# Kernel optimization log

Measured on AMD Instinct MI355X. Metric: run time of the kernel, lower is better.

## Reference

```python
import jax, jax.numpy as jnp
import numpy as np

NUM_EXPERTS = 64
TOP_K = 2
DIM = 4096
TOKENS = 16384


def setup_inputs() -> dict:
    key = jax.random.key(0)
    k1, k2 = jax.random.split(key)
    x = jax.random.normal(k1, (TOKENS, DIM), dtype=jnp.float32)
    # nn.Linear weight: [num_experts, dim], scaled like kaiming-uniform-ish init
    w_gating = jax.random.normal(k2, (NUM_EXPERTS, DIM), dtype=jnp.float32) * (1.0 / np.sqrt(DIM))
    return {"x": x, "w_gating": w_gating}


def reference(x, w_gating):
    # gating linear (no bias, noise=0 / eval mode)
    logits = jnp.einsum("td,ed->te", x, w_gating)          # [tokens, experts]
    scores = jax.nn.softmax(logits, axis=-1)                # [tokens, experts]
    topk_scores, topk_experts = jax.lax.top_k(scores, TOP_K)  # [tokens, top_k]
    combine_weight = topk_scores
    me = scores.mean(axis=0)                                # [experts]
    ce = (scores > 0).astype(jnp.float32).mean(axis=0)      # [experts]
    load_balance_loss = (me * ce).sum() * NUM_EXPERTS
    z_loss = (jax.nn.logsumexp(logits, axis=-1) ** 2).mean()
    return topk_experts, combine_weight, scores, load_balance_loss, z_loss
```

## Files before the change

### kernel.cpp

```cpp
#include <hip/hip_runtime.h>
#include <hip/hip_bf16.h>

typedef __attribute__((ext_vector_type(8))) short bf16x8;
typedef __attribute__((ext_vector_type(4))) float f32x4;

#define N_TOKENS 16384
#define DIM 4096
#define TOKB 32
#define NIT 32
#define NBUF 4
#define BUF_F (16 * 256)
#define N_EXP 64

#define OFF_W   (N_TOKENS * 2)
#define OFF_S   (N_TOKENS * 4)
#define OFF_LBL (N_TOKENS * 4 + N_TOKENS * N_EXP)
#define OFF_Z   (OFF_LBL + 1)

#define WS_WHI_F 512
#define WS_WLO_F (512 + (N_EXP * DIM) / 2)

typedef const __attribute__((address_space(1))) void GV;
typedef __attribute__((address_space(3))) void LV;

__device__ __forceinline__ unsigned int pkhi(float a, float b) {
  return __builtin_amdgcn_perm(__float_as_uint(b), __float_as_uint(a), 0x07060302u);
}
__device__ __forceinline__ float resid(float f) {
  return f - __uint_as_float(__float_as_uint(f) & 0xFFFF0000u);
}
__device__ __forceinline__ void tsplit8(const f32x4 p0, const f32x4 p1,
                                        bf16x8& hi, bf16x8& lo) {
  uint4 H = make_uint4(pkhi(p0[0], p0[1]), pkhi(p0[2], p0[3]),
                       pkhi(p1[0], p1[1]), pkhi(p1[2], p1[3]));
  float r0 = resid(p0[0]), r1 = resid(p0[1]), r2 = resid(p0[2]), r3 = resid(p0[3]);
  float r4 = resid(p1[0]), r5 = resid(p1[1]), r6 = resid(p1[2]), r7 = resid(p1[3]);
  uint4 L = make_uint4(pkhi(r0, r1), pkhi(r2, r3), pkhi(r4, r5), pkhi(r6, r7));
  hi = __builtin_bit_cast(bf16x8, H);
  lo = __builtin_bit_cast(bf16x8, L);
}

__global__ __launch_bounds__(256) void split_w_kernel(
    const float* __restrict__ w,
    unsigned short* __restrict__ whi, unsigned short* __restrict__ wlo)
{
  const int i = blockIdx.x * 256 + threadIdx.x;
  const int e = i >> 12, k = i & 4095;
  float f = w[i];
  unsigned short h = __builtin_bit_cast(unsigned short, __float2bfloat16(f));
  float hf = __uint_as_float(((unsigned)h) << 16);
  unsigned short l = __builtin_bit_cast(unsigned short, __float2bfloat16(f - hf));
  const int q = e >> 5, n = (e >> 4) & 1, r15 = e & 15;
  const int kc = k >> 8, kq = (k >> 6) & 3, j = (k >> 5) & 1, half = (k >> 3) & 3,
            jj = k & 7;
  const int lane = half * 16 + r15;
  const int idx = ((kq * 2 + q) << 15) + kc * 2048 + (j * 2 + n) * 512 + lane * 8 + jj;
  whi[idx] = h;
  wlo[idx] = l;
}

__global__ __launch_bounds__(512, 4) void router_kernel(
    const float* __restrict__ x,
    const unsigned short* __restrict__ whi, const unsigned short* __restrict__ wlo,
    float* __restrict__ out, float* __restrict__ ws)
{
  __shared__ __align__(16) float smem[NBUF * BUF_F];

  const int tid  = threadIdx.x;
  const int lane = tid & 63;
  const int wv   = __builtin_amdgcn_readfirstlane(tid >> 6);
  const int q    = wv & 1;
  const int kq   = wv >> 1;
  const int half = lane >> 4;
  const int r15  = lane & 15;
  const int g8   = r15 & 7;
  const int tok0 = blockIdx.x * TOKB;

  const int rl0 = 2 * wv, rl1 = 2 * wv + 1;
  const float* gs00 = x + (size_t)(tok0 + rl0) * DIM      + ((lane ^ (rl0 & 7)) << 2);
  const float* gs01 = x + (size_t)(tok0 + rl1) * DIM      + ((lane ^ (rl1 & 7)) << 2);
  const float* gs10 = x + (size_t)(tok0 + 16 + rl0) * DIM + ((lane ^ (rl0 & 7)) << 2);
  const float* gs11 = x + (size_t)(tok0 + 16 + rl1) * DIM + ((lane ^ (rl1 & 7)) << 2);
  float* const ldst = smem + wv * 512;

#define STAGE(buf, it_) do {                                                  \
    const int rh_ = (it_) & 1;                                                \
    const size_t ko_ = (size_t)((it_) >> 1) * 256;                            \
    const float* s0_ = (rh_ ? gs10 : gs00) + ko_;                             \
    const float* s1_ = (rh_ ? gs11 : gs01) + ko_;                             \
    float* d_ = ldst + (buf) * BUF_F;                                         \
    __builtin_amdgcn_global_load_lds((GV*)s0_, (LV*)d_,       16, 0, 0);      \
    __builtin_amdgcn_global_load_lds((GV*)s1_, (LV*)(d_+256), 16, 0, 0);      \
  } while (0)

  const unsigned short* wph = whi + ((kq * 2 + q) << 15);
  const unsigned short* wpl = wlo + ((kq * 2 + q) << 15);
  const int lo16 = lane * 8;

  f32x4 acc0[2], acc1[2];
#pragma unroll
  for (int n = 0; n < 2; ++n) {
    acc0[n] = (f32x4){0.f, 0.f, 0.f, 0.f};
    acc1[n] = (f32x4){0.f, 0.f, 0.f, 0.f};
  }

#define COMPUTE(itc, ACC, H00, H01, H10, H11, L00, L01, L10, L11) do {         \
    const float* rp = smem + ((itc) & 3) * BUF_F + r15 * 256;                  \
     {                                                              \
      const int u0 = kq * 16 + ((half * 2) ^ g8);                              \
      const int u1 = kq * 16 + ((half * 2 + 1) ^ g8);                          \
      f32x4 p0 = *(const f32x4*)(rp + (u0 << 2));                              \
      f32x4 p1 = *(const f32x4*)(rp + (u1 << 2));                              \
      bf16x8 ah, al;                                                           \
      tsplit8(p0, p1, ah, al);                                                 \
      ACC[0] = __builtin_amdgcn_mfma_f32_16x16x32_bf16(ah, H00, ACC[0], 0, 0, 0); \
      ACC[0] = __builtin_amdgcn_mfma_f32_16x16x32_bf16(al, H00, ACC[0], 0, 0, 0); \
      ACC[0] = __builtin_amdgcn_mfma_f32_16x16x32_bf16(ah, L00, ACC[0], 0, 0, 0); \
      ACC[1] = __builtin_amdgcn_mfma_f32_16x16x32_bf16(ah, H01, ACC[1], 0, 0, 0); \
      ACC[1] = __builtin_amdgcn_mfma_f32_16x16x32_bf16(al, H01, ACC[1], 0, 0, 0); \
      ACC[1] = __builtin_amdgcn_mfma_f32_16x16x32_bf16(ah, L01, ACC[1], 0, 0, 0); \
    }                                                                          \
     {                                                              \
      const int u0 = kq * 16 + 8 + ((half * 2) ^ g8);                          \
      const int u1 = kq * 16 + 8 + ((half * 2 + 1) ^ g8);                      \
      f32x4 p0 = *(const f32x4*)(rp + (u0 << 2));                              \
      f32x4 p1 = *(const f32x4*)(rp + (u1 << 2));                              \
      bf16x8 ah, al;                                                           \
      tsplit8(p0, p1, ah, al);                                                 \
      ACC[0] = __builtin_amdgcn_mfma_f32_16x16x32_bf16(ah, H10, ACC[0], 0, 0, 0); \
      ACC[0] = __builtin_amdgcn_mfma_f32_16x16x32_bf16(al, H10, ACC[0], 0, 0, 0); \
      ACC[0] = __builtin_amdgcn_mfma_f32_16x16x32_bf16(ah, L10, ACC[0], 0, 0, 0); \
      ACC[1] = __builtin_amdgcn_mfma_f32_16x16x32_bf16(ah, H11, ACC[1], 0, 0, 0); \
      ACC[1] = __builtin_amdgcn_mfma_f32_16x16x32_bf16(al, H11, ACC[1], 0, 0, 0); \
      ACC[1] = __builtin_amdgcn_mfma_f32_16x16x32_bf16(ah, L11, ACC[1], 0, 0, 0); \
    }                                                                          \
  } while (0)

  STAGE(0, 0);
  STAGE(1, 1);

  for (int s = 0; s < NIT / 2; ++s) {
    const int it0 = 2 * s, it1 = 2 * s + 1;

    const unsigned short* ph = wph + s * 2048;
    const unsigned short* pl = wpl + s * 2048;
    bf16x8 H00 = *(const bf16x8*)(ph + lo16);
    bf16x8 H01 = *(const bf16x8*)(ph + 512 + lo16);
    bf16x8 H10 = *(const bf16x8*)(ph + 1024 + lo16);
    bf16x8 H11 = *(const bf16x8*)(ph + 1536 + lo16);
    bf16x8 L00 = *(const bf16x8*)(pl + lo16);
    bf16x8 L01 = *(const bf16x8*)(pl + 512 + lo16);
    bf16x8 L10 = *(const bf16x8*)(pl + 1024 + lo16);
    bf16x8 L11 = *(const bf16x8*)(pl + 1536 + lo16);

    STAGE((it0 + 2) & 3, (it0 + 2 < NIT) ? it0 + 2 : NIT - 1);

    asm volatile("s_waitcnt vmcnt(12)" ::: "memory");
    __builtin_amdgcn_s_barrier();
    COMPUTE(it0, acc0, H00, H01, H10, H11, L00, L01, L10, L11);

    STAGE((it1 + 2) & 3, (it1 + 2 < NIT) ? it1 + 2 : NIT - 1);
    asm volatile("s_waitcnt vmcnt(4)" ::: "memory");
    __builtin_amdgcn_s_barrier();
    COMPUTE(it1, acc1, H00, H01, H10, H11, L00, L01, L10, L11);
  }

  asm volatile("s_waitcnt vmcnt(0)" ::: "memory");
  __syncthreads();

  float* lb = smem;
  {
    float* dst = lb + kq * (TOKB * 65);
#pragma unroll
    for (int n = 0; n < 2; ++n) {
#pragma unroll
      for (int r = 0; r < 4; ++r) {
        dst[(half * 4 + r) * 65 + q * 32 + n * 16 + r15]      = acc0[n][r];
        dst[(16 + half * 4 + r) * 65 + q * 32 + n * 16 + r15] = acc1[n][r];
      }
    }
  }
  __syncthreads();

  for (int i = tid; i < TOKB * 64; i += 512) {
    const int t = i >> 6, e = i & 63;
    lb[t * 65 + e] += lb[2080 + t * 65 + e] + lb[4160 + t * 65 + e] + lb[6240 + t * 65 + e];
  }
  __syncthreads();

  if (wv == 0 && lane < TOKB) {
    const int token = tok0 + lane;
    float v[64];
#pragma unroll
    for (int e = 0; e < 64; ++e) v[e] = lb[lane * 65 + e];
    float m = v[0];
#pragma unroll
    for (int e = 1; e < 64; ++e) m = fmaxf(m, v[e]);
    float sum = 0.f;
#pragma unroll
    for (int e = 0; e < 64; ++e) { v[e] = expf(v[e] - m); sum += v[e]; }
    const float inv = 1.0f / sum;
    float m1 = -1.f, m2 = -1.f;
    int   i1 = 0,    i2 = 0;
#pragma unroll
    for (int e = 0; e < 64; ++e) {
      float sc = v[e] * inv;
      lb[lane * 65 + e] = sc;
      if (sc > m1)      { m2 = m1; i2 = i1; m1 = sc; i1 = e; }
      else if (sc > m2) { m2 = sc; i2 = e; }
    }
    out[2 * token]         = (float)i1;
    out[2 * token + 1]     = (float)i2;
    out[OFF_W + 2 * token]     = m1;
    out[OFF_W + 2 * token + 1] = m2;

    float lse = m + logf(sum);
    float z = lse * lse;
#pragma unroll
    for (int off = 16; off > 0; off >>= 1) z += __shfl_down(z, off);
    if (lane == 0) atomicAdd(ws + 128, z);
  }
  __syncthreads();

  float* outS = out + OFF_S + (size_t)blockIdx.x * TOKB * 64;
  for (int i = tid; i < TOKB * 64; i += 512) {
    outS[i] = lb[(i >> 6) * 65 + (i & 63)];
  }

  if (wv == 0) {
    float sm = 0.f, cn = 0.f;
#pragma unroll
    for (int t = 0; t < TOKB; ++t) {
      float sc = lb[t * 65 + lane];
      sm += sc;
      cn += (sc > 0.f) ? 1.f : 0.f;
    }
    atomicAdd(ws + lane, sm);
    atomicAdd(ws + 64 + lane, cn);
  }
#undef STAGE
#undef COMPUTE
}

__global__ void finalize_kernel(const float* __restrict__ ws, float* __restrict__ out) {
  const int l = threadIdx.x;
  const float invT = 1.0f / (float)N_TOKENS;
  float me = ws[l] * invT;
  float ce = ws[64 + l] * invT;
  float p = me * ce;
#pragma unroll
  for (int off = 32; off > 0; off >>= 1) p += __shfl_down(p, off);
  if (l == 0) {
    out[OFF_LBL] = p * (float)N_EXP;
    out[OFF_Z]   = ws[128] * invT;
  }
}

extern "C" void kernel_launch(void* const* d_in, const int* in_sizes, int n_in,
                              void* d_out, int out_size, void* d_ws, size_t ws_size,
                              hipStream_t stream) {
  const float* x = (const float*)d_in[0];
  const float* w = (const float*)d_in[1];
  float* out = (float*)d_out;
  float* ws  = (float*)d_ws;
  unsigned short* whi = (unsigned short*)(ws + WS_WHI_F);
  unsigned short* wlo = (unsigned short*)(ws + WS_WLO_F);

  (void)hipMemsetAsync(d_ws, 0, 129 * sizeof(float), stream);
  split_w_kernel<<<(N_EXP * DIM) / 256, 256, 0, stream>>>(w, whi, wlo);
  router_kernel<<<N_TOKENS / TOKB, 512, 0, stream>>>(x, whi, wlo, out, ws);
  finalize_kernel<<<1, 64, 0, stream>>>(ws, out);
}
```

Before: 81.78 us.

## Fuse memset and finalize into kernels, vectorize weight split

Removes the hipMemsetAsync by zeroing the accumulator workspace inside split_w_kernel, and removes the finalize kernel by having the last router block (detected via an atomic counter) compute the load-balance and z losses. split_w_kernel now processes 8 weights per thread with vector loads and 16-byte stores. This cuts two launches and makes the weight split more memory-efficient, at the cost of an extra barrier and an atomic per router block.

New measurement: 92.33 us. 12.9% more time.

```diff
diff --git a/kernel.cpp b/kernel.cpp
--- a/kernel.cpp
+++ b/kernel.cpp
@@ -11,6 +11,7 @@
 #define NBUF 4
 #define BUF_F (16 * 256)
 #define N_EXP 64
+#define NBLK (N_TOKENS / TOKB)
 
 #define OFF_W   (N_TOKENS * 2)
 #define OFF_S   (N_TOKENS * 4)
@@ -42,21 +43,35 @@
 
 __global__ __launch_bounds__(256) void split_w_kernel(
     const float* __restrict__ w,
-    unsigned short* __restrict__ whi, unsigned short* __restrict__ wlo)
+    unsigned short* __restrict__ whi, unsigned short* __restrict__ wlo,
+    float* __restrict__ ws)
 {
-  const int i = blockIdx.x * 256 + threadIdx.x;
-  const int e = i >> 12, k = i & 4095;
-  float f = w[i];
-  unsigned short h = __builtin_bit_cast(unsigned short, __float2bfloat16(f));
-  float hf = __uint_as_float(((unsigned)h) << 16);
-  unsigned short l = __builtin_bit_cast(unsigned short, __float2bfloat16(f - hf));
+  if (blockIdx.x == 0 && threadIdx.x < 130) ws[threadIdx.x] = 0.0f;
+
+  const int i8 = blockIdx.x * 256 + threadIdx.x;
+  const int base = i8 * 8;
+  const int e = base >> 12, k0 = base & 4095;
   const int q = e >> 5, n = (e >> 4) & 1, r15 = e & 15;
-  const int kc = k >> 8, kq = (k >> 6) & 3, j = (k >> 5) & 1, half = (k >> 3) & 3,
-            jj = k & 7;
+  const int kc = k0 >> 8, kq = (k0 >> 6) & 3, j = (k0 >> 5) & 1, half = (k0 >> 3) & 3;
   const int lane = half * 16 + r15;
-  const int idx = ((kq * 2 + q) << 15) + kc * 2048 + (j * 2 + n) * 512 + lane * 8 + jj;
-  whi[idx] = h;
-  wlo[idx] = l;
+  const int idx = ((kq * 2 + q) << 15) + kc * 2048 + (j * 2 + n) * 512 + lane * 8;
+
+  f32x4 a = *(const f32x4*)(w + base);
+  f32x4 b = *(const f32x4*)(w + base + 4);
+  bf16x8 hi, lo;
+  short h[8], l[8];
+#pragma unroll
+  for (int t = 0; t < 8; ++t) {
+    float f = (t < 4) ? a[t] : b[t - 4];
+    unsigned short hh = __builtin_bit_cast(unsigned short, __float2bfloat16(f));
+    float hf = __uint_as_float(((unsigned)hh) << 16);
+    unsigned short ll = __builtin_bit_cast(unsigned short, __float2bfloat16(f - hf));
+    h[t] = (short)hh; l[t] = (short)ll;
+  }
+#pragma unroll
+  for (int t = 0; t < 8; ++t) { hi[t] = h[t]; lo[t] = l[t]; }
+  *(bf16x8*)(whi + idx) = hi;
+  *(bf16x8*)(wlo + idx) = lo;
 }
 
 __global__ __launch_bounds__(512, 4) void router_kernel(
@@ -65,6 +80,7 @@
     float* __restrict__ out, float* __restrict__ ws)
 {
   __shared__ __align__(16) float smem[NBUF * BUF_F];
+  __shared__ unsigned last_flag;
 
   const int tid  = threadIdx.x;
   const int lane = tid & 63;
@@ -238,22 +254,29 @@
     atomicAdd(ws + lane, sm);
     atomicAdd(ws + 64 + lane, cn);
   }
+
+  __syncthreads();
+  if (tid == 0) {
+    __threadfence();
+    unsigned t = atomicAdd((unsigned int*)(ws + 129), 1u);
+    last_flag = (t == NBLK - 1) ? 1u : 0u;
+  }
+  __syncthreads();
+  if (last_flag && wv == 0) {
+    const float invT = 1.0f / (float)N_TOKENS;
+    float me = atomicAdd(ws + lane, 0.0f) * invT;
+    float ce = atomicAdd(ws + 64 + lane, 0.0f) * invT;
+    float p = me * ce;
+#pragma unroll
+    for (int off = 32; off > 0; off >>= 1) p += __shfl_down(p, off);
+    if (lane == 0) {
+      float z = atomicAdd(ws + 128, 0.0f);
+      out[OFF_LBL] = p * (float)N_EXP;
+      out[OFF_Z]   = z * invT;
+    }
+  }
 #undef STAGE
 #undef COMPUTE
-}
-
-__global__ void finalize_kernel(const float* __restrict__ ws, float* __restrict__ out) {
-  const int l = threadIdx.x;
-  const float invT = 1.0f / (float)N_TOKENS;
-  float me = ws[l] * invT;
-  float ce = ws[64 + l] * invT;
-  float p = me * ce;
-#pragma unroll
-  for (int off = 32; off > 0; off >>= 1) p += __shfl_down(p, off);
-  if (l == 0) {
-    out[OFF_LBL] = p * (float)N_EXP;
-    out[OFF_Z]   = ws[128] * invT;
-  }
 }
 
 extern "C" void kernel_launch(void* const* d_in, const int* in_sizes, int n_in,
@@ -266,8 +289,6 @@
   unsigned short* whi = (unsigned short*)(ws + WS_WHI_F);
   unsigned short* wlo = (unsigned short*)(ws + WS_WLO_F);
 
-  (void)hipMemsetAsync(d_ws, 0, 129 * sizeof(float), stream);
-  split_w_kernel<<<(N_EXP * DIM) / 256, 256, 0, stream>>>(w, whi, wlo);
-  router_kernel<<<N_TOKENS / TOKB, 512, 0, stream>>>(x, whi, wlo, out, ws);
-  finalize_kernel<<<1, 64, 0, stream>>>(ws, out);
-}
+  split_w_kernel<<<(N_EXP * DIM) / 8 / 256, 256, 0, stream>>>(w, whi, wlo, ws);
+  router_kernel<<<NBLK, 512, 0, stream>>>(x, whi, wlo, out, ws);
+}
```
